# Kernel optimization log

Measured on AMD Instinct MI355X. Metric: run time of the kernel, lower is better.

## Reference

```python
import jax, jax.numpy as jnp
import numpy as np

N_NODES = 100000
N_EDGES = 1200000
NFEAT = 64
NHID = 64
NCLASS = 16
BN_EPS = 1e-5
L2_EPS = 1e-12


def setup_inputs() -> dict:
    key = jax.random.key(0)
    ks = jax.random.split(key, 8)
    edge_index = jax.random.randint(ks[0], (2, N_EDGES), 0, N_NODES, dtype=jnp.int64)
    x = jax.random.normal(ks[1], (N_NODES, NFEAT), dtype=jnp.float32)
    # SAGEConv params: lin_l (neighbor path, has bias), lin_r (root path, no bias)
    W_l = jax.random.normal(ks[2], (NHID, NFEAT), dtype=jnp.float32) * (1.0 / np.sqrt(NFEAT))
    b_l = jnp.zeros((NHID,), dtype=jnp.float32)
    W_r = jax.random.normal(ks[3], (NHID, NFEAT), dtype=jnp.float32) * (1.0 / np.sqrt(NFEAT))
    # BatchNorm1d affine params
    gamma = jnp.ones((NHID,), dtype=jnp.float32)
    beta = jnp.zeros((NHID,), dtype=jnp.float32)
    # final fc (xavier-ish scale, zero bias per weights_init)
    W_fc = jax.random.normal(ks[4], (NCLASS, NHID), dtype=jnp.float32) * (1.0 / np.sqrt(NHID))
    b_fc = jnp.zeros((NCLASS,), dtype=jnp.float32)
    return {"edge_index": edge_index, "x": x, "W_l": W_l, "b_l": b_l,
            "W_r": W_r, "gamma": gamma, "beta": beta, "W_fc": W_fc, "b_fc": b_fc}


def reference(edge_index, x, W_l, b_l, W_r, gamma, beta, W_fc, b_fc):
    N = x.shape[0]
    src, dst = edge_index[0], edge_index[1]
    # SAGEConv mean aggregation: gather x at source nodes, scatter-mean to dst
    msgs = x[src]                                                  # [E, F]
    sums = jax.ops.segment_sum(msgs, dst, num_segments=N)         # [N, F]
    cnt = jax.ops.segment_sum(jnp.ones((src.shape[0], 1), x.dtype), dst, num_segments=N)
    mean = sums / jnp.maximum(cnt, 1.0)
    # out = lin_l(mean_neighbors) + lin_r(x_root)
    h = mean @ W_l.T + b_l + x @ W_r.T                              # [N, H]
    # normalize=True -> L2 normalize rows (F.normalize semantics)
    h = h / jnp.maximum(jnp.linalg.norm(h, axis=-1, keepdims=True), L2_EPS)
    # transition: ReLU -> BatchNorm1d (training stats) -> Dropout (identity in eval)
    h = jax.nn.relu(h)
    mu = jnp.mean(h, axis=0)
    var = jnp.var(h, axis=0)
    h = (h - mu) / jnp.sqrt(var + BN_EPS) * gamma + beta
    return h @ W_fc.T + b_fc                                        # [N, C]
```

## Files before the change

kernel.cpp:

```cpp
#include <hip/hip_runtime.h>
#include <hip/hip_bf16.h>


typedef __attribute__((ext_vector_type(8))) short short8;
typedef __attribute__((ext_vector_type(4))) float f32x4;

__device__ __forceinline__ unsigned short f2bf(float f) {
    unsigned int u = __builtin_bit_cast(unsigned int, f);
    u += 0x7FFFu + ((u >> 16) & 1u);
    return (unsigned short)(u >> 16);
}
__device__ __forceinline__ float bf2f(unsigned short s) {
    return __builtin_bit_cast(float, ((unsigned int)s) << 16);
}

#define CHUNK 8192

__global__ __launch_bounds__(256) void k_prep(const int* __restrict__ eidx,
                                              int* __restrict__ cnt,
                                              const float4* __restrict__ x4,
                                              ushort4* __restrict__ xbf,
                                              int E, int NB, int NBLK,
                                              int n4, int do_x) {
    __shared__ int lh[256];
    const int tid = threadIdx.x;
    if ((int)blockIdx.x < NBLK) {
        lh[tid] = 0;
        __syncthreads();
        const int base = blockIdx.x * CHUNK;
        for (int i = tid; i < CHUNK; i += 256) {
            int e = base + i;
            if (e < E) atomicAdd(&lh[eidx[E + e] >> 9], 1);
        }
        __syncthreads();
        if (tid < NB) cnt[(size_t)tid * NBLK + blockIdx.x] = lh[tid];
    } else if (do_x) {
        int t = ((int)blockIdx.x - NBLK) * 256 + tid;
        if (t < n4) {
            float4 v = x4[t];
            xbf[t] = make_ushort4(f2bf(v.x), f2bf(v.y), f2bf(v.z), f2bf(v.w));
        }
    }
}

__global__ __launch_bounds__(256) void k_scanbkt(int* __restrict__ cnt,
                                                 int* __restrict__ btot,
                                                 int NBLK) {
    __shared__ int swv[4];
    const int b = blockIdx.x;
    const int t = threadIdx.x;
    int v = (t < NBLK) ? cnt[(size_t)b * NBLK + t] : 0;
    const int lane = t & 63, wid = t >> 6;
    int s = v;
#pragma unroll
    for (int off = 1; off < 64; off <<= 1) {
        int tt = __shfl_up(s, off);
        if (lane >= off) s += tt;
    }
    if (lane == 63) swv[wid] = s;
    __syncthreads();
    if (t == 0) {
        int a = 0;
#pragma unroll
        for (int w = 0; w < 4; ++w) { int tt = swv[w]; swv[w] = a; a += tt; }
    }
    __syncthreads();
    int excl = s - v + swv[wid];
    if (t < NBLK) cnt[(size_t)b * NBLK + t] = excl;
    if (t == 255) btot[b] = swv[3] + s;
}

__global__ __launch_bounds__(256) void k_bscanB(const int* __restrict__ btot,
                                                int* __restrict__ bbase,
                                                int* __restrict__ rowptr,
                                                int NB, int N, int E) {
    __shared__ int swv[4];
    const int t = threadIdx.x;
    int v = (t < NB) ? btot[t] : 0;
    const int lane = t & 63, wid = t >> 6;
    int s = v;
#pragma unroll
    for (int off = 1; off < 64; off <<= 1) {
        int tt = __shfl_up(s, off);
        if (lane >= off) s += tt;
    }
    if (lane == 63) swv[wid] = s;
    __syncthreads();
    if (t == 0) {
        int a = 0;
#pragma unroll
        for (int w = 0; w < 4; ++w) { int tt = swv[w]; swv[w] = a; a += tt; }
    }
    __syncthreads();
    if (t < NB) bbase[t] = s - v + swv[wid];
    if (t == 0) { bbase[NB] = E; rowptr[N] = E; }
}

__global__ __launch_bounds__(256) void k_bscatter(const int* __restrict__ eidx,
                                                  const int* __restrict__ cnt,
                                                  const int* __restrict__ bbase,
                                                  unsigned int* __restrict__ ebuf,
                                                  int E, int NB, int NBLK) {
    __shared__ int cur[256];
    const int tid = threadIdx.x;
    if (tid < NB)
        cur[tid] = bbase[tid] + cnt[(size_t)tid * NBLK + blockIdx.x];
    __syncthreads();
    const int base = blockIdx.x * CHUNK;
    for (int i = tid; i < CHUNK; i += 256) {
        int e = base + i;
        if (e < E) {
            int d = eidx[E + e];
            int s = eidx[e];
            int p = atomicAdd(&cur[d >> 9], 1);
            ebuf[p] = (unsigned int)s | ((unsigned int)(d & 511) << 17);
        }
    }
}

__global__ __launch_bounds__(256) void k_bfinal(const unsigned int* __restrict__ ebuf,
                                                const int* __restrict__ bbase,
                                                int* __restrict__ rowptr,
                                                int* __restrict__ colv, int N) {
    __shared__ int h[512];
    __shared__ int swv[4];
    const int b = blockIdx.x;
    const int tid = threadIdx.x;
    h[2 * tid] = 0;
    h[2 * tid + 1] = 0;
    __syncthreads();
    const int segb = bbase[b], sege = bbase[b + 1];
    for (int i = segb + tid; i < sege; i += 256)
        atomicAdd(&h[ebuf[i] >> 17], 1);
    __syncthreads();
    int a0 = h[2 * tid], a1 = h[2 * tid + 1];
    int ts = a0 + a1;
    const int lane = tid & 63, wid = tid >> 6;
    int s = ts;
#pragma unroll
    for (int off = 1; off < 64; off <<= 1) {
        int tt = __shfl_up(s, off);
        if (lane >= off) s += tt;
    }
    if (lane == 63) swv[wid] = s;
    __syncthreads();
    if (tid == 0) {
        int a = 0;
#pragma unroll
        for (int w = 0; w < 4; ++w) { int tt = swv[w]; swv[w] = a; a += tt; }
    }
    __syncthreads();
    int excl = s - ts + swv[wid];
    h[2 * tid] = excl;
    h[2 * tid + 1] = excl + a0;
    int node = b * 512 + 2 * tid;
    if (node < N) rowptr[node] = segb + excl;
    if (node + 1 < N) rowptr[node + 1] = segb + excl + a0;
    __syncthreads();
    for (int i = segb + tid; i < sege; i += 256) {
        unsigned int u = ebuf[i];
        int p = atomicAdd(&h[u >> 17], 1);
        colv[segb + p] = (int)(u & 0x1FFFFu);
    }
}

__global__ __launch_bounds__(256) void k_gather_bf(
        const uint2* __restrict__ xbf2, const int* __restrict__ rowptr,
        const int* __restrict__ colv, uint2* __restrict__ mh2, int N) {
    int t = blockIdx.x * 256 + threadIdx.x;
    int n = t >> 4;
    int l = t & 15;
    if (n >= N) return;
    int b = rowptr[n], e = rowptr[n + 1];
    float a0 = 0.f, a1 = 0.f, a2 = 0.f, a3 = 0.f;
    int p = b;
    for (; p + 4 <= e; p += 4) {
        int s0 = colv[p], s1 = colv[p + 1], s2 = colv[p + 2], s3 = colv[p + 3];
        uint2 v0 = xbf2[(size_t)s0 * 16 + l];
        uint2 v1 = xbf2[(size_t)s1 * 16 + l];
        uint2 v2 = xbf2[(size_t)s2 * 16 + l];
        uint2 v3 = xbf2[(size_t)s3 * 16 + l];
        a0 += bf2f((unsigned short)(v0.x & 0xFFFF)) + bf2f((unsigned short)(v1.x & 0xFFFF)) +
              bf2f((unsigned short)(v2.x & 0xFFFF)) + bf2f((unsigned short)(v3.x & 0xFFFF));
        a1 += bf2f((unsigned short)(v0.x >> 16)) + bf2f((unsigned short)(v1.x >> 16)) +
              bf2f((unsigned short)(v2.x >> 16)) + bf2f((unsigned short)(v3.x >> 16));
        a2 += bf2f((unsigned short)(v0.y & 0xFFFF)) + bf2f((unsigned short)(v1.y & 0xFFFF)) +
              bf2f((unsigned short)(v2.y & 0xFFFF)) + bf2f((unsigned short)(v3.y & 0xFFFF));
        a3 += bf2f((unsigned short)(v0.y >> 16)) + bf2f((unsigned short)(v1.y >> 16)) +
              bf2f((unsigned short)(v2.y >> 16)) + bf2f((unsigned short)(v3.y >> 16));
    }
    for (; p < e; ++p) {
        int s0 = colv[p];
        uint2 v0 = xbf2[(size_t)s0 * 16 + l];
        a0 += bf2f((unsigned short)(v0.x & 0xFFFF));
        a1 += bf2f((unsigned short)(v0.x >> 16));
        a2 += bf2f((unsigned short)(v0.y & 0xFFFF));
        a3 += bf2f((unsigned short)(v0.y >> 16));
    }
    float inv = 1.0f / fmaxf((float)(e - b), 1.0f);
    uint2 o;
    o.x = (unsigned int)f2bf(a0 * inv) | ((unsigned int)f2bf(a1 * inv) << 16);
    o.y = (unsigned int)f2bf(a2 * inv) | ((unsigned int)f2bf(a3 * inv) << 16);
    mh2[(size_t)n * 16 + l] = o;
}

__global__ __launch_bounds__(256) void k_gather_f32(
        const float4* __restrict__ x4, const int* __restrict__ rowptr,
        const int* __restrict__ colv, ushort4* __restrict__ mh, int N) {
    int t = blockIdx.x * 256 + threadIdx.x;
    int n = t >> 4;
    int l = t & 15;
    if (n >= N) return;
    int b = rowptr[n], e = rowptr[n + 1];
    float ax = 0.f, ay = 0.f, az = 0.f, aw = 0.f;
    int p = b;
    for (; p + 4 <= e; p += 4) {
        int s0 = colv[p], s1 = colv[p + 1], s2 = colv[p + 2], s3 = colv[p + 3];
        float4 v0 = x4[(size_t)s0 * 16 + l];
        float4 v1 = x4[(size_t)s1 * 16 + l];
        float4 v2 = x4[(size_t)s2 * 16 + l];
        float4 v3 = x4[(size_t)s3 * 16 + l];
        ax += (v0.x + v1.x) + (v2.x + v3.x);
        ay += (v0.y + v1.y) + (v2.y + v3.y);
        az += (v0.z + v1.z) + (v2.z + v3.z);
        aw += (v0.w + v1.w) + (v2.w + v3.w);
    }
    for (; p < e; ++p) {
        int s0 = colv[p];
        float4 v0 = x4[(size_t)s0 * 16 + l];
        ax += v0.x; ay += v0.y; az += v0.z; aw += v0.w;
    }
    float inv = 1.0f / fmaxf((float)(e - b), 1.0f);
    mh[(size_t)n * 16 + l] = make_ushort4(f2bf(ax * inv), f2bf(ay * inv),
                                          f2bf(az * inv), f2bf(aw * inv));
}

__global__ __launch_bounds__(256) void k_fused(
        const float* __restrict__ x,
        const unsigned short* __restrict__ xbf, int use_bf,
        const float* __restrict__ Wl, const float* __restrict__ bl,
        const float* __restrict__ Wr,
        unsigned short* __restrict__ mh,
        float* __restrict__ pstats, int N) {
    __shared__ float sRed[4][128];

    const int tid = threadIdx.x;
    const int wid = tid >> 6;
    const int lane = tid & 63;
    const int l15 = lane & 15;
    const int quad = lane >> 4;

    short8 bfrag[4][4];
#pragma unroll
    for (int c = 0; c < 4; ++c) {
#pragma unroll
        for (int f = 0; f < 4; ++f) {
            const int n = f * 16 + l15;
            const float* wsrc = (c < 2)
                ? (Wl + (size_t)n * 64 + c * 32 + quad * 8)
                : (Wr + (size_t)n * 64 + (c - 2) * 32 + quad * 8);
            float4 w0 = *(const float4*)wsrc;
            float4 w1 = *(const float4*)(wsrc + 4);
            union { short8 v; unsigned short u[8]; } pk;
            pk.u[0] = f2bf(w0.x); pk.u[1] = f2bf(w0.y);
            pk.u[2] = f2bf(w0.z); pk.u[3] = f2bf(w0.w);
            pk.u[4] = f2bf(w1.x); pk.u[5] = f2bf(w1.y);
            pk.u[6] = f2bf(w1.z); pk.u[7] = f2bf(w1.w);
            bfrag[c][f] = pk.v;
        }
    }

    float blv[4];
#pragma unroll
    for (int f = 0; f < 4; ++f) blv[f] = bl[f * 16 + l15];

    float psum[4] = {0.f, 0.f, 0.f, 0.f};
    float psq[4] = {0.f, 0.f, 0.f, 0.f};

    for (int t4 = 0; t4 < 4; ++t4) {
        const int tbase = blockIdx.x * 256 + wid * 64 + t4 * 16;
        const int mrow = tbase + l15;
        const int mld = (mrow < N) ? mrow : (N - 1);
        f32x4 acc[4] = {{0.f, 0.f, 0.f, 0.f}, {0.f, 0.f, 0.f, 0.f},
                        {0.f, 0.f, 0.f, 0.f}, {0.f, 0.f, 0.f, 0.f}};
#pragma unroll
        for (int c = 0; c < 2; ++c) {
            short8 a = *(const short8*)(mh + (size_t)mld * 64 + c * 32 + quad * 8);
#pragma unroll
            for (int f = 0; f < 4; ++f)
                acc[f] = __builtin_amdgcn_mfma_f32_16x16x32_bf16(a, bfrag[c][f], acc[f], 0, 0, 0);
        }
        if (use_bf) {
#pragma unroll
            for (int c = 0; c < 2; ++c) {
                short8 a = *(const short8*)(xbf + (size_t)mld * 64 + c * 32 + quad * 8);
#pragma unroll
                for (int f = 0; f < 4; ++f)
                    acc[f] = __builtin_amdgcn_mfma_f32_16x16x32_bf16(a, bfrag[c + 2][f], acc[f], 0, 0, 0);
            }
        } else {
#pragma unroll
            for (int c = 0; c < 2; ++c) {
                const float* xp = x + (size_t)mld * 64 + c * 32 + quad * 8;
                float4 a0 = *(const float4*)xp;
                float4 a1 = *(const float4*)(xp + 4);
                union { short8 v; unsigned short u[8]; } pk;
                pk.u[0] = f2bf(a0.x); pk.u[1] = f2bf(a0.y);
                pk.u[2] = f2bf(a0.z); pk.u[3] = f2bf(a0.w);
                pk.u[4] = f2bf(a1.x); pk.u[5] = f2bf(a1.y);
                pk.u[6] = f2bf(a1.z); pk.u[7] = f2bf(a1.w);
#pragma unroll
                for (int f = 0; f < 4; ++f)
                    acc[f] = __builtin_amdgcn_mfma_f32_16x16x32_bf16(pk.v, bfrag[c + 2][f], acc[f], 0, 0, 0);
            }
        }

#pragma unroll
        for (int reg = 0; reg < 4; ++reg) {
            const int node = tbase + quad * 4 + reg;
            float hv[4];
            float ss = 0.f;
#pragma unroll
            for (int f = 0; f < 4; ++f) {
                hv[f] = acc[f][reg] + blv[f];
                ss += hv[f] * hv[f];
            }
            ss += __shfl_xor(ss, 1);
            ss += __shfl_xor(ss, 2);
            ss += __shfl_xor(ss, 4);
            ss += __shfl_xor(ss, 8);
            float sc = 1.0f / fmaxf(sqrtf(ss), 1e-12f);
            if (node < N) {
#pragma unroll
                for (int f = 0; f < 4; ++f) {
                    float r = fmaxf(hv[f] * sc, 0.f);
                    unsigned short rb = f2bf(r);
                    float e = bf2f(rb);
                    mh[(size_t)node * 64 + f * 16 + l15] = rb;
                    psum[f] += e;
                    psq[f] += e * e;
                }
            }
        }
    }

#pragma unroll
    for (int f = 0; f < 4; ++f) {
        psum[f] += __shfl_xor(psum[f], 16);
        psum[f] += __shfl_xor(psum[f], 32);
        psq[f] += __shfl_xor(psq[f], 16);
        psq[f] += __shfl_xor(psq[f], 32);
    }
    if (lane < 16) {
#pragma unroll
        for (int f = 0; f < 4; ++f) {
            sRed[wid][f * 16 + l15] = psum[f];
            sRed[wid][64 + f * 16 + l15] = psq[f];
        }
    }
    __syncthreads();
    if (tid < 128) {
        float v = sRed[0][tid] + sRed[1][tid] + sRed[2][tid] + sRed[3][tid];
        pstats[(size_t)blockIdx.x * 128 + tid] = v;
    }
}

__global__ __launch_bounds__(64) void k_stats(const float* __restrict__ pstats,
                                              float* __restrict__ stats, int nblk) {
    int col = blockIdx.x;
    int l = threadIdx.x;
    float s = 0.f;
    for (int r = l; r < nblk; r += 64) s += pstats[(size_t)r * 128 + col];
    s += __shfl_xor(s, 1);
    s += __shfl_xor(s, 2);
    s += __shfl_xor(s, 4);
    s += __shfl_xor(s, 8);
    s += __shfl_xor(s, 16);
    s += __shfl_xor(s, 32);
    if (l == 0) stats[col] = s;
}

__global__ __launch_bounds__(256) void k_out(
        const unsigned short* __restrict__ h, const float* __restrict__ stats,
        const float* __restrict__ gamma, const float* __restrict__ beta,
        const float* __restrict__ Wfc, const float* __restrict__ bfc,
        float* __restrict__ out, int N) {
    __shared__ float sWm[64 * 16];
    __shared__ float sShift[64];
    __shared__ float sBase[16];
    const int tid = threadIdx.x;
    const float invN = 1.0f / (float)N;
    if (tid < 64) {
        float mu = stats[tid] * invN;
        float var = stats[64 + tid] * invN - mu * mu;
        float sc = gamma[tid] / sqrtf(var + 1e-5f);
        sShift[tid] = beta[tid] - mu * sc;
#pragma unroll
        for (int c = 0; c < 16; ++c) sWm[tid * 16 + c] = Wfc[c * 64 + tid] * sc;
    }
    __syncthreads();
    if (tid < 16) {
        float b = bfc[tid];
#pragma unroll
        for (int j = 0; j < 64; ++j) b += sShift[j] * Wfc[tid * 64 + j];
        sBase[tid] = b;
    }
    __syncthreads();
    int g = blockIdx.x * 256 + tid;
    int n = g >> 4;
    int c = g & 15;
    if (n >= N) return;
    const ushort4* h4 = (const ushort4*)(h + (size_t)n * 64);
    float acc = sBase[c];
#pragma unroll
    for (int jq = 0; jq < 16; ++jq) {
        ushort4 v = h4[jq];
        acc += bf2f(v.x) * sWm[(jq * 4 + 0) * 16 + c];
        acc += bf2f(v.y) * sWm[(jq * 4 + 1) * 16 + c];
        acc += bf2f(v.z) * sWm[(jq * 4 + 2) * 16 + c];
        acc += bf2f(v.w) * sWm[(jq * 4 + 3) * 16 + c];
    }
    out[(size_t)n * 16 + c] = acc;
}

extern "C" void kernel_launch(void* const* d_in, const int* in_sizes, int n_in,
                              void* d_out, int out_size, void* d_ws, size_t ws_size,
                              hipStream_t stream) {
    const int* eidx = (const int*)d_in[0];
    const float* x = (const float*)d_in[1];
    const float* Wl = (const float*)d_in[2];
    const float* bl = (const float*)d_in[3];
    const float* Wr = (const float*)d_in[4];
    const float* gamma = (const float*)d_in[5];
    const float* beta = (const float*)d_in[6];
    const float* Wfc = (const float*)d_in[7];
    const float* bfc = (const float*)d_in[8];
    float* out = (float*)d_out;

    const int E = in_sizes[0] / 2;
    const int N = in_sizes[1] / 64;
    const int NB = (N + 511) >> 9;
    const int NBLK = (E + CHUNK - 1) / CHUNK;
    const int fb2 = (N + 255) / 256;
    const int n4 = N * 16;

    int* cnt = (int*)d_ws;
    int* btot = cnt + (size_t)NB * NBLK;
    int* bbase = btot + NB;
    int* rowptr = bbase + NB + 1;
    float* pstats = (float*)(rowptr + N + 1);
    float* stats = pstats + (size_t)fb2 * 128;
    int* colv = (int*)(stats + 128);
    unsigned int* ebuf = (unsigned int*)(colv + E);
    unsigned short* mh = (unsigned short*)(ebuf + E);
    unsigned short* xbf = mh + (size_t)N * 64;

    size_t need_bf = (size_t)((char*)(xbf + (size_t)N * 64) - (char*)d_ws);
    const int use_bf = (ws_size >= need_bf) ? 1 : 0;

    int cbl = use_bf ? (n4 + 255) / 256 : 0;
    k_prep<<<NBLK + cbl, 256, 0, stream>>>(eidx, cnt, (const float4*)x,
                                           (ushort4*)xbf, E, NB, NBLK, n4, use_bf);
    k_scanbkt<<<NB, 256, 0, stream>>>(cnt, btot, NBLK);
    k_bscanB<<<1, 256, 0, stream>>>(btot, bbase, rowptr, NB, N, E);
    k_bscatter<<<NBLK, 256, 0, stream>>>(eidx, cnt, bbase, ebuf, E, NB, NBLK);
    k_bfinal<<<NB, 256, 0, stream>>>(ebuf, bbase, rowptr, colv, N);

    int gblocks = (int)(((size_t)N * 16 + 255) / 256);
    if (use_bf) {
        k_gather_bf<<<gblocks, 256, 0, stream>>>((const uint2*)xbf, rowptr, colv,
                                                 (uint2*)mh, N);
    } else {
        k_gather_f32<<<gblocks, 256, 0, stream>>>((const float4*)x, rowptr, colv,
                                                  (ushort4*)mh, N);
    }

    k_fused<<<fb2, 256, 0, stream>>>(x, xbf, use_bf, Wl, bl, Wr, mh, pstats, N);
    k_stats<<<128, 64, 0, stream>>>(pstats, stats, fb2);

    int oblocks = (int)(((size_t)N * 16 + 255) / 256);
    k_out<<<oblocks, 256, 0, stream>>>(mh, stats, gamma, beta, Wfc, bfc, out, N);
}
```

Before: 216.1 us.

## Fold bucket-base scan into consumers, stage scatter in LDS, widen gather loads

Removes the single-block bucket-base scan kernel. Each bscatter and bfinal block now recomputes the prefix over bucket totals in shared memory, which saves one launch and a serialization point. The bucket scatter first sorts each chunk locally in LDS (32KB of staging) and then writes contiguous runs per bucket to global memory, replacing scattered global writes with coalesced ones. The bf16 gather now uses 16-byte loads with 8 lanes per node instead of 8-byte loads with 16 lanes, giving fewer memory requests but more accumulator registers per thread.

```diff
diff --git a/kernel.cpp b/kernel.cpp
--- a/kernel.cpp
+++ b/kernel.cpp
@@ -15,6 +15,25 @@
 }
 
 #define CHUNK 8192
+
+__device__ __forceinline__ int scan256(int v, int* swv) {
+    const int lane = threadIdx.x & 63, wid = threadIdx.x >> 6;
+    int s = v;
+#pragma unroll
+    for (int off = 1; off < 64; off <<= 1) {
+        int t = __shfl_up(s, off);
+        if (lane >= off) s += t;
+    }
+    if (lane == 63) swv[wid] = s;
+    __syncthreads();
+    if (threadIdx.x == 0) {
+        int a = 0;
+#pragma unroll
+        for (int w = 0; w < 4; ++w) { int t = swv[w]; swv[w] = a; a += t; }
+    }
+    __syncthreads();
+    return s - v + swv[wid];
+}
 
 __global__ __launch_bounds__(256) void k_prep(const int* __restrict__ eidx,
                                               int* __restrict__ cnt,
@@ -50,107 +69,96 @@
     const int b = blockIdx.x;
     const int t = threadIdx.x;
     int v = (t < NBLK) ? cnt[(size_t)b * NBLK + t] : 0;
-    const int lane = t & 63, wid = t >> 6;
-    int s = v;
-#pragma unroll
-    for (int off = 1; off < 64; off <<= 1) {
-        int tt = __shfl_up(s, off);
-        if (lane >= off) s += tt;
-    }
-    if (lane == 63) swv[wid] = s;
-    __syncthreads();
-    if (t == 0) {
-        int a = 0;
-#pragma unroll
-        for (int w = 0; w < 4; ++w) { int tt = swv[w]; swv[w] = a; a += tt; }
-    }
-    __syncthreads();
-    int excl = s - v + swv[wid];
+    int excl = scan256(v, swv);
     if (t < NBLK) cnt[(size_t)b * NBLK + t] = excl;
-    if (t == 255) btot[b] = swv[3] + s;
-}
-
-__global__ __launch_bounds__(256) void k_bscanB(const int* __restrict__ btot,
-                                                int* __restrict__ bbase,
-                                                int* __restrict__ rowptr,
-                                                int NB, int N, int E) {
-    __shared__ int swv[4];
-    const int t = threadIdx.x;
-    int v = (t < NB) ? btot[t] : 0;
-    const int lane = t & 63, wid = t >> 6;
-    int s = v;
-#pragma unroll
-    for (int off = 1; off < 64; off <<= 1) {
-        int tt = __shfl_up(s, off);
-        if (lane >= off) s += tt;
-    }
-    if (lane == 63) swv[wid] = s;
-    __syncthreads();
-    if (t == 0) {
-        int a = 0;
-#pragma unroll
-        for (int w = 0; w < 4; ++w) { int tt = swv[w]; swv[w] = a; a += tt; }
-    }
-    __syncthreads();
-    if (t < NB) bbase[t] = s - v + swv[wid];
-    if (t == 0) { bbase[NB] = E; rowptr[N] = E; }
+    if (t == 255) btot[b] = excl + v;
 }
 
 __global__ __launch_bounds__(256) void k_bscatter(const int* __restrict__ eidx,
                                                   const int* __restrict__ cnt,
-                                                  const int* __restrict__ bbase,
+                                                  const int* __restrict__ btot,
                                                   unsigned int* __restrict__ ebuf,
                                                   int E, int NB, int NBLK) {
-    __shared__ int cur[256];
+    __shared__ int bb[257];
+    __shared__ int lbeg[256];
+    __shared__ int lcur[256];
+    __shared__ unsigned int stag[CHUNK];
+    __shared__ int swv[4];
     const int tid = threadIdx.x;
-    if (tid < NB)
-        cur[tid] = bbase[tid] + cnt[(size_t)tid * NBLK + blockIdx.x];
-    __syncthreads();
-    const int base = blockIdx.x * CHUNK;
+    const int c = blockIdx.x;
+
+    {
+        int v = (tid < NB) ? btot[tid] : 0;
+        int excl = scan256(v, swv);
+        if (tid < NB) bb[tid] = excl;
+        if (tid == NB - 1) bb[NB] = excl + v;
+    }
+    lcur[tid] = 0;
+    __syncthreads();
+    const int base = c * CHUNK;
+    for (int i = tid; i < CHUNK; i += 256) {
+        int e = base + i;
+        if (e < E) atomicAdd(&lcur[eidx[E + e] >> 9], 1);
+    }
+    __syncthreads();
+    {
+        int v = lcur[tid];
+        __syncthreads();
+        int excl = scan256(v, swv);
+        lbeg[tid] = excl;
+        __syncthreads();
+        lcur[tid] = excl;
+    }
+    __syncthreads();
     for (int i = tid; i < CHUNK; i += 256) {
         int e = base + i;
         if (e < E) {
             int d = eidx[E + e];
             int s = eidx[e];
-            int p = atomicAdd(&cur[d >> 9], 1);
-            ebuf[p] = (unsigned int)s | ((unsigned int)(d & 511) << 17);
-        }
+            int p = atomicAdd(&lcur[d >> 9], 1);
+            stag[p] = (unsigned int)s | ((unsigned int)(d & 511) << 17);
+        }
+    }
+    __syncthreads();
+    const int wid = tid >> 6, lane = tid & 63;
+    for (int b = wid; b < NB; b += 4) {
+        int lo = lbeg[b];
+        int hi = lcur[b];
+        int gbase = bb[b] + cnt[(size_t)b * NBLK + c];
+        for (int i = lo + lane; i < hi; i += 64)
+            ebuf[gbase + (i - lo)] = stag[i];
     }
 }
 
 __global__ __launch_bounds__(256) void k_bfinal(const unsigned int* __restrict__ ebuf,
-                                                const int* __restrict__ bbase,
+                                                const int* __restrict__ btot,
                                                 int* __restrict__ rowptr,
-                                                int* __restrict__ colv, int N) {
+                                                int* __restrict__ colv,
+                                                int N, int NB, int E) {
+    __shared__ int bb[257];
     __shared__ int h[512];
     __shared__ int swv[4];
     const int b = blockIdx.x;
     const int tid = threadIdx.x;
+
+    {
+        int v = (tid < NB) ? btot[tid] : 0;
+        int excl = scan256(v, swv);
+        if (tid < NB) bb[tid] = excl;
+        if (tid == NB - 1) bb[NB] = excl + v;
+    }
     h[2 * tid] = 0;
     h[2 * tid + 1] = 0;
     __syncthreads();
-    const int segb = bbase[b], sege = bbase[b + 1];
+    const int segb = bb[b], sege = bb[b + 1];
+    if (b == 0 && tid == 0) rowptr[N] = E;
     for (int i = segb + tid; i < sege; i += 256)
         atomicAdd(&h[ebuf[i] >> 17], 1);
     __syncthreads();
     int a0 = h[2 * tid], a1 = h[2 * tid + 1];
     int ts = a0 + a1;
-    const int lane = tid & 63, wid = tid >> 6;
-    int s = ts;
-#pragma unroll
-    for (int off = 1; off < 64; off <<= 1) {
-        int tt = __shfl_up(s, off);
-        if (lane >= off) s += tt;
-    }
-    if (lane == 63) swv[wid] = s;
-    __syncthreads();
-    if (tid == 0) {
-        int a = 0;
-#pragma unroll
-        for (int w = 0; w < 4; ++w) { int tt = swv[w]; swv[w] = a; a += tt; }
-    }
-    __syncthreads();
-    int excl = s - ts + swv[wid];
+    __syncthreads();
+    int excl = scan256(ts, swv);
     h[2 * tid] = excl;
     h[2 * tid + 1] = excl + a0;
     int node = b * 512 + 2 * tid;
@@ -165,43 +173,57 @@
 }
 
 __global__ __launch_bounds__(256) void k_gather_bf(
-        const uint2* __restrict__ xbf2, const int* __restrict__ rowptr,
-        const int* __restrict__ colv, uint2* __restrict__ mh2, int N) {
+        const uint4* __restrict__ xbf4, const int* __restrict__ rowptr,
+        const int* __restrict__ colv, uint4* __restrict__ mh4, int N) {
     int t = blockIdx.x * 256 + threadIdx.x;
-    int n = t >> 4;
-    int l = t & 15;
+    int n = t >> 3;
+    int l = t & 7;
     if (n >= N) return;
     int b = rowptr[n], e = rowptr[n + 1];
-    float a0 = 0.f, a1 = 0.f, a2 = 0.f, a3 = 0.f;
+    float a[8] = {0.f, 0.f, 0.f, 0.f, 0.f, 0.f, 0.f, 0.f};
     int p = b;
     for (; p + 4 <= e; p += 4) {
         int s0 = colv[p], s1 = colv[p + 1], s2 = colv[p + 2], s3 = colv[p + 3];
-        uint2 v0 = xbf2[(size_t)s0 * 16 + l];
-        uint2 v1 = xbf2[(size_t)s1 * 16 + l];
-        uint2 v2 = xbf2[(size_t)s2 * 16 + l];
-        uint2 v3 = xbf2[(size_t)s3 * 16 + l];
-        a0 += bf2f((unsigned short)(v0.x & 0xFFFF)) + bf2f((unsigned short)(v1.x & 0xFFFF)) +
-              bf2f((unsigned short)(v2.x & 0xFFFF)) + bf2f((unsigned short)(v3.x & 0xFFFF));
-        a1 += bf2f((unsigned short)(v0.x >> 16)) + bf2f((unsigned short)(v1.x >> 16)) +
-              bf2f((unsigned short)(v2.x >> 16)) + bf2f((unsigned short)(v3.x >> 16));
-        a2 += bf2f((unsigned short)(v0.y & 0xFFFF)) + bf2f((unsigned short)(v1.y & 0xFFFF)) +
-              bf2f((unsigned short)(v2.y & 0xFFFF)) + bf2f((unsigned short)(v3.y & 0xFFFF));
-        a3 += bf2f((unsigned short)(v0.y >> 16)) + bf2f((unsigned short)(v1.y >> 16)) +
-              bf2f((unsigned short)(v2.y >> 16)) + bf2f((unsigned short)(v3.y >> 16));
+        uint4 v0 = xbf4[(size_t)s0 * 8 + l];
+        uint4 v1 = xbf4[(size_t)s1 * 8 + l];
+        uint4 v2 = xbf4[(size_t)s2 * 8 + l];
+        uint4 v3 = xbf4[(size_t)s3 * 8 + l];
+        unsigned int w0[4] = {v0.x, v0.y, v0.z, v0.w};
+        unsigned int w1[4] = {v1.x, v1.y, v1.z, v1.w};
+        unsigned int w2[4] = {v2.x, v2.y, v2.z, v2.w};
+        unsigned int w3[4] = {v3.x, v3.y, v3.z, v3.w};
+#pragma unroll
+        for (int q = 0; q < 4; ++q) {
+            a[2 * q] += bf2f((unsigned short)(w0[q] & 0xFFFF)) +
+                        bf2f((unsigned short)(w1[q] & 0xFFFF)) +
+                        bf2f((unsigned short)(w2[q] & 0xFFFF)) +
+                        bf2f((unsigned short)(w3[q] & 0xFFFF));
+            a[2 * q + 1] += bf2f((unsigned short)(w0[q] >> 16)) +
+                            bf2f((unsigned short)(w1[q] >> 16)) +
+                            bf2f((unsigned short)(w2[q] >> 16)) +
+                            bf2f((unsigned short)(w3[q] >> 16));
+        }
     }
     for (; p < e; ++p) {
         int s0 = colv[p];
-        uint2 v0 = xbf2[(size_t)s0 * 16 + l];
-        a0 += bf2f((unsigned short)(v0.x & 0xFFFF));
-        a1 += bf2f((unsigned short)(v0.x >> 16));
-        a2 += bf2f((unsigned short)(v0.y & 0xFFFF));
-        a3 += bf2f((unsigned short)(v0.y >> 16));
+        uint4 v0 = xbf4[(size_t)s0 * 8 + l];
+        unsigned int w0[4] = {v0.x, v0.y, v0.z, v0.w};
+#pragma unroll
+        for (int q = 0; q < 4; ++q) {
+            a[2 * q] += bf2f((unsigned short)(w0[q] & 0xFFFF));
+            a[2 * q + 1] += bf2f((unsigned short)(w0[q] >> 16));
+        }
     }
     float inv = 1.0f / fmaxf((float)(e - b), 1.0f);
-    uint2 o;
-    o.x = (unsigned int)f2bf(a0 * inv) | ((unsigned int)f2bf(a1 * inv) << 16);
-    o.y = (unsigned int)f2bf(a2 * inv) | ((unsigned int)f2bf(a3 * inv) << 16);
-    mh2[(size_t)n * 16 + l] = o;
+    uint4 o;
+    unsigned int* op = &o.x;
+#pragma unroll
+    for (int q = 0; q < 4; ++q) {
+        unsigned int lo = f2bf(a[2 * q] * inv);
+        unsigned int hi = f2bf(a[2 * q + 1] * inv);
+        op[q] = lo | (hi << 16);
+    }
+    mh4[(size_t)n * 8 + l] = o;
 }
 
 __global__ __launch_bounds__(256) void k_gather_f32(
@@ -446,8 +468,7 @@
 
     int* cnt = (int*)d_ws;
     int* btot = cnt + (size_t)NB * NBLK;
-    int* bbase = btot + NB;
-    int* rowptr = bbase + NB + 1;
+    int* rowptr = btot + NB;
     float* pstats = (float*)(rowptr + N + 1);
     float* stats = pstats + (size_t)fb2 * 128;
     int* colv = (int*)(stats + 128);
@@ -462,15 +483,15 @@
     k_prep<<<NBLK + cbl, 256, 0, stream>>>(eidx, cnt, (const float4*)x,
                                            (ushort4*)xbf, E, NB, NBLK, n4, use_bf);
     k_scanbkt<<<NB, 256, 0, stream>>>(cnt, btot, NBLK);
-    k_bscanB<<<1, 256, 0, stream>>>(btot, bbase, rowptr, NB, N, E);
-    k_bscatter<<<NBLK, 256, 0, stream>>>(eidx, cnt, bbase, ebuf, E, NB, NBLK);
-    k_bfinal<<<NB, 256, 0, stream>>>(ebuf, bbase, rowptr, colv, N);
-
-    int gblocks = (int)(((size_t)N * 16 + 255) / 256);
+    k_bscatter<<<NBLK, 256, 0, stream>>>(eidx, cnt, btot, ebuf, E, NB, NBLK);
+    k_bfinal<<<NB, 256, 0, stream>>>(ebuf, btot, rowptr, colv, N, NB, E);
+
     if (use_bf) {
-        k_gather_bf<<<gblocks, 256, 0, stream>>>((const uint2*)xbf, rowptr, colv,
-                                                 (uint2*)mh, N);
+        int gblocks = (int)(((size_t)N * 8 + 255) / 256);
+        k_gather_bf<<<gblocks, 256, 0, stream>>>((const uint4*)xbf, rowptr, colv,
+                                                 (uint4*)mh, N);
     } else {
+        int gblocks = (int)(((size_t)N * 16 + 255) / 256);
         k_gather_f32<<<gblocks, 256, 0, stream>>>((const float4*)x, rowptr, colv,
                                                   (ushort4*)mh, N);
     }
```

Result: slower. 235.1 us (+8.8%).
